# Optimization experiments

Measured on AMD Instinct MI355X. Metric: run time of the kernel, lower is better.

Reference implementation:

```python
import jax, jax.numpy as jnp
import numpy as np

N = 100000      # nodes
D = 128         # embed_dim == hidden_size (code forces them equal)
M = 3           # edge_types / meta-paths
L = 2           # layers
E = 1600000     # edges per meta-path (avg degree 16)
ATT = 128       # semantic attention hidden size


def setup_inputs():
    key = jax.random.key(0)
    ks = jax.random.split(key, 8)
    x = jnp.arange(N)
    edge_index0 = jax.random.randint(ks[0], (2, E), 0, N)
    edge_index1 = jax.random.randint(ks[1], (2, E), 0, N)
    edge_index2 = jax.random.randint(ks[2], (2, E), 0, N)
    embed_table = jax.random.normal(ks[3], (N, D), dtype=jnp.float32) * 0.02
    W = jax.random.normal(ks[4], (L, M, D, D), dtype=jnp.float32) / np.sqrt(D)
    B = jnp.zeros((L, M, D), dtype=jnp.float32)
    att_w1 = jax.random.normal(ks[5], (L, D, ATT), dtype=jnp.float32) / np.sqrt(D)
    att_b1 = jnp.zeros((L, ATT), dtype=jnp.float32)
    att_w2 = jax.random.normal(ks[6], (L, ATT, 1), dtype=jnp.float32) / np.sqrt(ATT)
    return dict(x=x, edge_index0=edge_index0, edge_index1=edge_index1,
                edge_index2=edge_index2, embed_table=embed_table, W=W, B=B,
                att_w1=att_w1, att_b1=att_b1, att_w2=att_w2)


def _gcn_conv(h, W, b, src, dst):
    # GCNConv(normalize=True): self-loops already appended to src/dst.
    deg = jax.ops.segment_sum(jnp.ones_like(dst, dtype=h.dtype), dst, num_segments=N)
    dinv = jnp.where(deg > 0, jax.lax.rsqrt(deg), 0.0)
    norm = dinv[src] * dinv[dst]                       # [E+N]
    hw = h @ W                                         # [N, D]
    msg = hw[src] * norm[:, None]                      # gather + scale
    return jax.ops.segment_sum(msg, dst, num_segments=N) + b


def reference(x, edge_index0, edge_index1, edge_index2,
              embed_table, W, B, att_w1, att_b1, att_w2):
    edges = [edge_index0, edge_index1, edge_index2]
    loops = jnp.arange(N)
    srcs = [jnp.concatenate([e[0], loops]) for e in edges]
    dsts = [jnp.concatenate([e[1], loops]) for e in edges]

    h = embed_table[x]                                 # [N, D]
    for l in range(L):
        sems = [_gcn_conv(h, W[l, m], B[l, m], srcs[m], dsts[m]) for m in range(M)]
        z = jnp.stack(sems, axis=1)                    # [N, M, D]
        # semantic attention: Linear -> tanh -> Linear(no bias), softmax over M
        w = jnp.tanh(z @ att_w1[l] + att_b1[l]) @ att_w2[l]   # [N, M, 1]
        beta = jax.nn.softmax(w, axis=1)
        h = (beta * z).sum(axis=1)                     # [N, D]
    return jax.nn.log_softmax(h, axis=1)
```

## Files before the change

### kernel.cpp

```cpp
#include <hip/hip_runtime.h>
#include <hip/hip_bf16.h>

#define NN 100000
#define DD 128
#define MM 3
#define EE 1600000
#define CH_NODES 512
#define NC ((NN + CH_NODES - 1) / CH_NODES)
#define ECAP 10752
#define ECHTOT ((size_t)NC * ECAP)
#define TILE_E 8192
#define NTILES ((EE + TILE_E - 1) / TILE_E)
#define DTILE 2048
#define NT2 ((NN + DTILE - 1) / DTILE)
#define NT2P 52
#define DBINS 512
#define HSCALE 64.0f
#define HINV (1.0f / 64.0f)
#define PADMARK 0xFFFFFFFFu

typedef unsigned int uint32_hip;
typedef short short8 __attribute__((ext_vector_type(8)));
typedef float floatx4 __attribute__((ext_vector_type(4)));
typedef float floatx2 __attribute__((ext_vector_type(2)));

__device__ __forceinline__ float bf2f(short s) {
  return __uint_as_float(((uint32_hip)(unsigned short)s) << 16);
}
__device__ __forceinline__ unsigned short f2bf(float f) {
  union { __hip_bfloat16 b; unsigned short u; } cv;
  cv.b = __float2bfloat16(f);
  return cv.u;
}
__device__ __forceinline__ uint32_hip packbf2(float x, float y) {
  return (uint32_hip)f2bf(x) | ((uint32_hip)f2bf(y) << 16);
}
__device__ __forceinline__ float tanh_apx(float x) {
  float e = __expf(2.0f * x);
  return 1.0f - 2.0f / (e + 1.0f);
}
__device__ __forceinline__ uint32_hip pack_fp8x4(float a, float b, float c, float d) {
  uint32_hip w = 0;
  w = __builtin_amdgcn_cvt_pk_fp8_f32(a, b, w, false);
  w = __builtin_amdgcn_cvt_pk_fp8_f32(c, d, w, true);
  return w;
}
__device__ __forceinline__ float h2f(uint32_hip u) {
  union { unsigned short us; _Float16 h; } cv;
  cv.us = (unsigned short)u;
  return (float)cv.h;
}
__device__ __forceinline__ unsigned short f2h(float f) {
  union { unsigned short us; _Float16 h; } cv;
  cv.h = (_Float16)f;
  return cv.us;
}
__device__ __forceinline__ void dec16(uint4 hv, floatx2* f) {
  f[0] = __builtin_amdgcn_cvt_pk_f32_fp8((int)hv.x, false);
  f[1] = __builtin_amdgcn_cvt_pk_f32_fp8((int)hv.x, true);
  f[2] = __builtin_amdgcn_cvt_pk_f32_fp8((int)hv.y, false);
  f[3] = __builtin_amdgcn_cvt_pk_f32_fp8((int)hv.y, true);
  f[4] = __builtin_amdgcn_cvt_pk_f32_fp8((int)hv.z, false);
  f[5] = __builtin_amdgcn_cvt_pk_f32_fp8((int)hv.z, true);
  f[6] = __builtin_amdgcn_cvt_pk_f32_fp8((int)hv.w, false);
  f[7] = __builtin_amdgcn_cvt_pk_f32_fp8((int)hv.w, true);
}

__global__ __launch_bounds__(256) void hist1_kernel(const int* __restrict__ e0,
                                                    const int* __restrict__ e1,
                                                    const int* __restrict__ e2,
                                                    int* __restrict__ thist) {
  __shared__ int hist[NC];
  int m = blockIdx.y, tile = blockIdx.x, t = threadIdx.x;
  const int* ei = (m == 0) ? e0 : (m == 1) ? e1 : e2;
  const int* dst = ei + EE;
  int beg = tile * TILE_E, end = min(beg + TILE_E, EE);
  if (t < NC) hist[t] = 0;
  __syncthreads();
  for (int e = beg + t; e < end; e += 256) atomicAdd(&hist[dst[e] >> 9], 1);
  __syncthreads();
  int* th = thist + (size_t)m * NC * NTILES + tile;
  if (t < NC) th[(size_t)t * NTILES] = hist[t];
}

__global__ __launch_bounds__(256) void scan1_kernel(int* __restrict__ thist,
                                                    int* __restrict__ ccount) {
  __shared__ int sw[256];
  int c = blockIdx.x, m = blockIdx.y, t = threadIdx.x;
  int* th = thist + ((size_t)m * NC + c) * NTILES;
  int v = (t < NTILES) ? th[t] : 0;
  sw[t] = v;
  __syncthreads();
  for (int off = 1; off < 256; off <<= 1) {
    int u = (t >= off) ? sw[t - off] : 0;
    __syncthreads();
    sw[t] += u;
    __syncthreads();
  }
  if (t < NTILES) th[t] = c * ECAP + sw[t] - v;
  if (t == NTILES - 1) ccount[m * NC + c] = sw[t];
}

__global__ __launch_bounds__(256) void scatter1_kernel(const int* __restrict__ e0,
                                                       const int* __restrict__ e1,
                                                       const int* __restrict__ e2,
                                                       const int* __restrict__ thist,
                                                       const int* __restrict__ ccount,
                                                       uint32_hip* __restrict__ lvl1) {
  __shared__ int gbase[NC];
  __shared__ int spos[NC];
  __shared__ int cur[NC];
  __shared__ int sw[256];
  __shared__ uint32_hip sval[TILE_E];
  __shared__ unsigned char sbuk[TILE_E];
  int m = blockIdx.y, tile = blockIdx.x, t = threadIdx.x;
  const int* ei = (m == 0) ? e0 : (m == 1) ? e1 : e2;
  const int* dst = ei + EE;
  const int* th = thist + (size_t)m * NC * NTILES + tile;
  int cnt = 0;
  if (t < NC) {
    int gb = th[(size_t)t * NTILES];
    int gn = (tile + 1 < NTILES) ? th[(size_t)t * NTILES + 1] : t * ECAP + ccount[m * NC + t];
    gbase[t] = gb;
    cnt = gn - gb;
  }
  sw[t] = cnt;
  __syncthreads();
  for (int off = 1; off < 256; off <<= 1) {
    int u = (t >= off) ? sw[t - off] : 0;
    __syncthreads();
    sw[t] += u;
    __syncthreads();
  }
  if (t < NC) {
    spos[t] = sw[t] - cnt;
    cur[t] = sw[t] - cnt;
  }
  __syncthreads();
  int beg = tile * TILE_E, end = min(beg + TILE_E, EE);
  int ct = end - beg;
  for (int e = beg + t; e < end; e += 256) {
    int s = ei[e], d = dst[e];
    int b = d >> 9;
    int r = atomicAdd(&cur[b], 1);
    sval[r] = (uint32_hip)s | ((uint32_hip)(d & 511) << 17);
    sbuk[r] = (unsigned char)b;
  }
  __syncthreads();
  uint32_hip* eb = lvl1 + (size_t)m * ECHTOT;
  for (int i = t; i < ct; i += 256) {
    int b = sbuk[i];
    eb[gbase[b] + (i - spos[b])] = sval[i];
  }
}

__global__ __launch_bounds__(256) void sort2_kernel(uint32_hip* __restrict__ lvl1,
                                                    const int* __restrict__ ccount,
                                                    int* __restrict__ astart,
                                                    unsigned short* __restrict__ sdeg,
                                                    int* __restrict__ cpad) {
  __shared__ uint32_hip ebl[ECAP];
  __shared__ int cnt[CH_NODES];
  __shared__ int pos[CH_NODES];
  __shared__ int sw[256];
  int m = blockIdx.y, c = blockIdx.x, t = threadIdx.x;
  int base = c * ECAP;
  int ct = ccount[m * NC + c];
  uint32_hip* eb = lvl1 + (size_t)m * ECHTOT + base;
  for (int e = t; e < ct; e += 256) ebl[e] = eb[e];
  cnt[t] = 0;
  cnt[t + 256] = 0;
  __syncthreads();
  for (int e = t; e < ct; e += 256) atomicAdd(&cnt[ebl[e] >> 17], 1);
  __syncthreads();
  int c0 = cnt[2 * t], c1 = cnt[2 * t + 1];
  int p0 = (c0 + 3) & ~3, p1 = (c1 + 3) & ~3;
  int s = p0 + p1;
  sw[t] = s;
  __syncthreads();
  for (int off = 1; off < 256; off <<= 1) {
    int u = (t >= off) ? sw[t - off] : 0;
    __syncthreads();
    sw[t] += u;
    __syncthreads();
  }
  int excl = sw[t] - s;
  pos[2 * t] = excl;
  pos[2 * t + 1] = excl + p0;
  int node0 = c * CH_NODES;
  {
    int n0 = node0 + 2 * t;
    if (n0 < NN) {
      astart[(size_t)m * NN + n0] = base + excl;
      sdeg[(size_t)m * NN + n0] = (unsigned short)c0;
    }
    int n1 = node0 + 2 * t + 1;
    if (n1 < NN) {
      astart[(size_t)m * NN + n1] = base + excl + p0;
      sdeg[(size_t)m * NN + n1] = (unsigned short)c1;
    }
  }
  if (t == 255) cpad[m * NC + c] = sw[255];
  __syncthreads();
  for (int e = t; e < ct; e += 256) {
    uint32_hip p = ebl[e];
    int q = atomicAdd(&pos[p >> 17], 1);
    eb[q] = p & 0x1FFFFu;
  }
  for (int i = c0; i < p0; ++i) eb[excl + i] = PADMARK;
  for (int i = c1; i < p1; ++i) eb[excl + p0 + i] = PADMARK;
}

__global__ void norm_embed_kernel(uint32_hip* __restrict__ lvl1, const int* __restrict__ cpad,
                                  const unsigned short* __restrict__ sdeg) {
  int m = blockIdx.y, c = blockIdx.x, t = threadIdx.x;
  int base = c * ECAP;
  int ct = cpad[m * NC + c];
  uint32_hip* eb = lvl1 + (size_t)m * ECHTOT + base;
  const unsigned short* sd = sdeg + (size_t)m * NN;
  for (int e = t; e < ct; e += 256) {
    uint32_hip p = eb[e];
    uint32_hip s = p & 0x1FFFFu;
    uint32_hip sc_ = (s < NN) ? s : 0;
    float dv = rsqrtf((float)(sd[sc_] + 1));
    eb[e] = (p == PADMARK) ? 0u : (s | ((uint32_hip)f2h(dv) << 17));
  }
}

__global__ __launch_bounds__(256) void dhist_kernel(const unsigned short* __restrict__ sdeg,
                                                    int* __restrict__ dthist) {
  __shared__ int hist[DBINS];
  int m = blockIdx.y, tile = blockIdx.x, t = threadIdx.x;
  const unsigned short* sd = sdeg + (size_t)m * NN;
  hist[t] = 0;
  hist[t + 256] = 0;
  __syncthreads();
  int beg = tile * DTILE, end = min(beg + DTILE, NN);
  for (int n = beg + t; n < end; n += 256) atomicAdd(&hist[min((int)sd[n], DBINS - 1)], 1);
  __syncthreads();
  int* th = dthist + ((size_t)m * DBINS) * NT2P + tile;
  th[(size_t)t * NT2P] = hist[t];
  th[(size_t)(t + 256) * NT2P] = hist[t + 256];
}

__global__ __launch_bounds__(64) void dscan_kernel(int* __restrict__ dthist,
                                                   int* __restrict__ bintot) {
  __shared__ int sw[64];
  int bin = blockIdx.x, m = blockIdx.y, t = threadIdx.x;
  int* th = dthist + ((size_t)m * DBINS + bin) * NT2P;
  int v = (t < NT2) ? th[t] : 0;
  sw[t] = v;
  __syncthreads();
  for (int off = 1; off < 64; off <<= 1) {
    int u = (t >= off) ? sw[t - off] : 0;
    __syncthreads();
    sw[t] += u;
    __syncthreads();
  }
  if (t < NT2) th[t] = sw[t] - v;
  if (t == 63) bintot[m * DBINS + bin] = sw[63];
}

__global__ __launch_bounds__(512) void dscan2_kernel(const int* __restrict__ bintot,
                                                     int* __restrict__ binbase) {
  __shared__ int sw[DBINS];
  int m = blockIdx.x, t = threadIdx.x;
  int v = bintot[m * DBINS + t];
  sw[t] = v;
  __syncthreads();
  for (int off = 1; off < DBINS; off <<= 1) {
    int u = (t >= off) ? sw[t - off] : 0;
    __syncthreads();
    sw[t] += u;
    __syncthreads();
  }
  binbase[m * DBINS + t] = sw[t] - v;
}

__global__ __launch_bounds__(256) void dscatter_kernel(const unsigned short* __restrict__ sdeg,
                                                       const int* __restrict__ astart,
                                                       const int* __restrict__ dthist,
                                                       const int* __restrict__ binbase,
                                                       uint2* __restrict__ pinfo) {
  __shared__ int cur[DBINS];
  int m = blockIdx.y, tile = blockIdx.x, t = threadIdx.x;
  const unsigned short* sd = sdeg + (size_t)m * NN;
  const int* as_ = astart + (size_t)m * NN;
  for (int b = t; b < DBINS; b += 256)
    cur[b] = binbase[m * DBINS + b] + dthist[((size_t)m * DBINS + b) * NT2P + tile];
  __syncthreads();
  uint2* pi = pinfo + (size_t)m * NN;
  int beg = tile * DTILE, end = min(beg + DTILE, NN);
  for (int n = beg + t; n < end; n += 256) {
    int d = sd[n];
    int r = atomicAdd(&cur[min(d, DBINS - 1)], 1);
    int slot = NN - 1 - r;
    uint2 v;
    v.x = (uint32_hip)as_[n];
    v.y = (uint32_hip)n | ((uint32_hip)d << 17);
    pi[slot] = v;
  }
}

__global__ void embed_kernel(const int* __restrict__ x, const float* __restrict__ tbl,
                             uint32_hip* __restrict__ hq) {
  int i = blockIdx.x * 256 + threadIdx.x;
  if (i < NN * 32) {
    int n = i >> 5;
    int c = i & 31;
    float4 v = ((const float4*)tbl)[(size_t)x[n] * 32 + c];
    hq[(size_t)n * 32 + c] =
        pack_fp8x4(v.x * HSCALE, v.y * HSCALE, v.z * HSCALE, v.w * HSCALE);
  }
}

__global__ __launch_bounds__(256) void agg_kernel(const uint32_hip* __restrict__ hq,
                                                  const uint2* __restrict__ pinfo,
                                                  const uint32_hip* __restrict__ csr,
                                                  uint32_hip* __restrict__ zall) {
  int m = blockIdx.y;
  const uint2* pi_ = pinfo + (size_t)m * NN;
  const uint32_hip* cs = csr + (size_t)m * ECHTOT;
  uint32_hip* zo = zall + (size_t)m * NN * 64;
  int t = threadIdx.x;
  int wave = t >> 6, lane = t & 63;
  int g = lane >> 3, l = lane & 7;
  int slot = blockIdx.x * 32 + wave * 8 + g;
  uint2 pi = pi_[slot];
  int e = (int)pi.x;
  int n = (int)(pi.y & 0x1FFFFu);
  int deg = (int)(pi.y >> 17);
  float di = rsqrtf((float)(deg + 1));
  floatx2 ac[8];
  {
    uint4 hv = *(const uint4*)(hq + (size_t)n * 32 + l * 4);
    floatx2 f[8];
    dec16(hv, f);
    floatx2 di2 = {di, di};
#pragma unroll
    for (int j = 0; j < 8; ++j) ac[j] = di2 * f[j];
  }
  int end = e + ((deg + 3) & ~3);
  uint4 ce = *(const uint4*)(cs + e);
  while (__any(e < end)) {
    int en = e + 4;
    uint4 cn = *(const uint4*)(cs + en);
    uint32_hip msk = (e < end) ? 0xFFFFFFFFu : 0u;
    uint32_hip cearr[4] = {ce.x & msk, ce.y & msk, ce.z & msk, ce.w & msk};
#pragma unroll
    for (int k = 0; k < 4; ++k) {
      uint32_hip ck = cearr[k];
      float nk = h2f(ck >> 17);
      int sk = ck & 0x1FFFF;
      uint4 hk = *(const uint4*)(hq + (size_t)sk * 32 + l * 4);
      floatx2 fk[8];
      dec16(hk, fk);
      floatx2 n2 = {nk, nk};
#pragma unroll
      for (int j = 0; j < 8; ++j) ac[j] = __builtin_elementwise_fma(n2, fk[j], ac[j]);
    }
    ce = cn;
    e = en;
  }
  float scv = di * HINV;
  floatx2 sc2 = {scv, scv};
#pragma unroll
  for (int j = 0; j < 8; ++j) ac[j] = ac[j] * sc2;
  uint4 w0, w1;
  w0.x = packbf2(ac[0].x, ac[0].y);
  w0.y = packbf2(ac[1].x, ac[1].y);
  w0.z = packbf2(ac[2].x, ac[2].y);
  w0.w = packbf2(ac[3].x, ac[3].y);
  w1.x = packbf2(ac[4].x, ac[4].y);
  w1.y = packbf2(ac[5].x, ac[5].y);
  w1.z = packbf2(ac[6].x, ac[6].y);
  w1.w = packbf2(ac[7].x, ac[7].y);
  uint32_hip* zr = zo + (size_t)n * 64 + l * 8;
  *(uint4*)zr = w0;
  *(uint4*)(zr + 4) = w1;
}

__global__ __launch_bounds__(256) void mfma_gemm_kernel(unsigned short* __restrict__ zall,
                                                        const float* __restrict__ Wall,
                                                        const float* __restrict__ Ball) {
  __shared__ unsigned short Wt[128 * 136];
  int m = blockIdx.y;
  const float* Wmat = Wall + (size_t)m * DD * DD;
  const float* bias = Ball + (size_t)m * DD;
  unsigned short* Z = zall + (size_t)m * NN * DD;
  int t = threadIdx.x;
  {
    uint32_hip* Wt_u = (uint32_hip*)Wt;
#pragma unroll
    for (int i = 0; i < 32; ++i) {
      int idx = i * 256 + t;
      int k2 = idx >> 7;
      int nn = idx & 127;
      float w0 = Wmat[(2 * k2) * 128 + nn];
      float w1 = Wmat[(2 * k2 + 1) * 128 + nn];
      Wt_u[nn * 68 + k2] = packbf2(w0, w1);
    }
  }
  __syncthreads();
  int wave = t >> 6, lane = t & 63;
  int quad = lane >> 4, ln = lane & 15;
  int rowbase = blockIdx.x * 64 + wave * 16;
  int arow = rowbase + ln;
  int arowc = (arow < NN) ? arow : (NN - 1);
  const short8* zrow = (const short8*)(Z + (size_t)arowc * 128);
  floatx4 acc[8];
#pragma unroll
  for (int c = 0; c < 8; ++c) acc[c] = (floatx4){0.f, 0.f, 0.f, 0.f};
#pragma unroll
  for (int kt = 0; kt < 4; ++kt) {
    short8 a = zrow[kt * 4 + quad];
#pragma unroll
    for (int c = 0; c < 8; ++c) {
      const short8* bp = (const short8*)(Wt + (c * 16 + ln) * 136 + kt * 32 + quad * 8);
      acc[c] = __builtin_amdgcn_mfma_f32_16x16x32_bf16(a, *bp, acc[c], 0, 0, 0);
    }
  }
#pragma unroll
  for (int c = 0; c < 8; ++c) {
    int col = c * 16 + ln;
    float bs = bias[col];
#pragma unroll
    for (int r = 0; r < 4; ++r) {
      int grow = rowbase + quad * 4 + r;
      if (grow < NN) Z[(size_t)grow * 128 + col] = f2bf(acc[c][r] + bs);
    }
  }
}

__global__ __launch_bounds__(256) void att_combine_kernel(
    const unsigned short* __restrict__ Z, const float* __restrict__ W1,
    const float* __restrict__ b1, const float* __restrict__ w2,
    uint32_hip* __restrict__ hq, float* __restrict__ fout, int last) {
  __shared__ unsigned short Wt[128 * 136];
  __shared__ float sc[4][3][16];
  int t = threadIdx.x;
  {
    uint32_hip* Wt_u = (uint32_hip*)Wt;
#pragma unroll
    for (int i = 0; i < 32; ++i) {
      int idx = i * 256 + t;
      int k2 = idx >> 7;
      int nn = idx & 127;
      float w0 = W1[(2 * k2) * 128 + nn];
      float w1 = W1[(2 * k2 + 1) * 128 + nn];
      Wt_u[nn * 68 + k2] = packbf2(w0, w1);
    }
  }
  __syncthreads();
  int wave = t >> 6, lane = t & 63;
  int quad = lane >> 4, ln = lane & 15;
  int nodebase = blockIdx.x * 64 + wave * 16;
  int frow = nodebase + ln;
  int frowc = (frow < NN) ? frow : (NN - 1);
  short8 af[3][4];
#pragma unroll
  for (int m = 0; m < 3; ++m) {
    const short8* zr = (const short8*)(Z + ((size_t)m * NN + frowc) * 128);
#pragma unroll
    for (int kt = 0; kt < 4; ++kt) af[m][kt] = zr[kt * 4 + quad];
  }
#pragma unroll
  for (int m = 0; m < 3; ++m) {
    floatx4 acc[8];
#pragma unroll
    for (int c = 0; c < 8; ++c) acc[c] = (floatx4){0.f, 0.f, 0.f, 0.f};
#pragma unroll
    for (int kt = 0; kt < 4; ++kt) {
#pragma unroll
      for (int c = 0; c < 8; ++c) {
        const short8* bp = (const short8*)(Wt + (c * 16 + ln) * 136 + kt * 32 + quad * 8);
        acc[c] = __builtin_amdgcn_mfma_f32_16x16x32_bf16(af[m][kt], *bp, acc[c], 0, 0, 0);
      }
    }
    float rows[4] = {0.f, 0.f, 0.f, 0.f};
#pragma unroll
    for (int c = 0; c < 8; ++c) {
      int col = c * 16 + ln;
      float bb = b1[col];
      float ww = w2[col];
#pragma unroll
      for (int r = 0; r < 4; ++r) rows[r] += tanh_apx(acc[c][r] + bb) * ww;
    }
#pragma unroll
    for (int off = 8; off > 0; off >>= 1) {
#pragma unroll
      for (int r = 0; r < 4; ++r) rows[r] += __shfl_down(rows[r], off);
    }
    if (ln == 0) {
#pragma unroll
      for (int r = 0; r < 4; ++r) sc[wave][m][quad * 4 + r] = rows[r];
    }
  }
  __syncthreads();
  float s0 = sc[wave][0][ln], s1 = sc[wave][1][ln], s2 = sc[wave][2][ln];
  float mx = fmaxf(s0, fmaxf(s1, s2));
  float e0 = __expf(s0 - mx), e1 = __expf(s1 - mx), e2 = __expf(s2 - mx);
  float inv = 1.0f / (e0 + e1 + e2);
  float bb0 = e0 * inv, bb1 = e1 * inv, bb2 = e2 * inv;
  float o[4][8];
#pragma unroll
  for (int kt = 0; kt < 4; ++kt) {
#pragma unroll
    for (int j = 0; j < 8; ++j) {
      o[kt][j] = bb0 * bf2f(af[0][kt][j]) + bb1 * bf2f(af[1][kt][j]) + bb2 * bf2f(af[2][kt][j]);
    }
  }
  if (!last) {
    if (frow < NN) {
#pragma unroll
      for (int kt = 0; kt < 4; ++kt) {
        uint2 v;
        v.x = pack_fp8x4(o[kt][0] * HSCALE, o[kt][1] * HSCALE, o[kt][2] * HSCALE,
                         o[kt][3] * HSCALE);
        v.y = pack_fp8x4(o[kt][4] * HSCALE, o[kt][5] * HSCALE, o[kt][6] * HSCALE,
                         o[kt][7] * HSCALE);
        *(uint2*)&hq[(size_t)frow * 32 + kt * 8 + quad * 2] = v;
      }
    }
  } else {
    float vmx = o[0][0];
#pragma unroll
    for (int kt = 0; kt < 4; ++kt)
#pragma unroll
      for (int j = 0; j < 8; ++j) vmx = fmaxf(vmx, o[kt][j]);
    vmx = fmaxf(vmx, __shfl_xor(vmx, 16));
    vmx = fmaxf(vmx, __shfl_xor(vmx, 32));
    float ss = 0.f;
#pragma unroll
    for (int kt = 0; kt < 4; ++kt)
#pragma unroll
      for (int j = 0; j < 8; ++j) ss += __expf(o[kt][j] - vmx);
    ss += __shfl_xor(ss, 16);
    ss += __shfl_xor(ss, 32);
    float lse = vmx + logf(ss);
    if (frow < NN) {
#pragma unroll
      for (int kt = 0; kt < 4; ++kt) {
        float4 a, b;
        a.x = o[kt][0] - lse; a.y = o[kt][1] - lse; a.z = o[kt][2] - lse; a.w = o[kt][3] - lse;
        b.x = o[kt][4] - lse; b.y = o[kt][5] - lse; b.z = o[kt][6] - lse; b.w = o[kt][7] - lse;
        float* dst = fout + (size_t)frow * 128 + kt * 32 + quad * 8;
        *(float4*)dst = a;
        *(float4*)(dst + 4) = b;
      }
    }
  }
}

extern "C" void kernel_launch(void* const* d_in, const int* in_sizes, int n_in,
                              void* d_out, int out_size, void* d_ws, size_t ws_size,
                              hipStream_t stream) {
  const int* x = (const int*)d_in[0];
  const int* e0 = (const int*)d_in[1];
  const int* e1 = (const int*)d_in[2];
  const int* e2 = (const int*)d_in[3];
  const float* embed = (const float*)d_in[4];
  const float* W = (const float*)d_in[5];
  const float* B = (const float*)d_in[6];
  const float* aw1 = (const float*)d_in[7];
  const float* ab1 = (const float*)d_in[8];
  const float* aw2 = (const float*)d_in[9];
  float* out = (float*)d_out;
  uint32_hip* hq = (uint32_hip*)d_out;

  char* ws = (char*)d_ws;
  size_t off = 0;
  auto alloc = [&](size_t bytes) {
    void* p = ws + off;
    off += (bytes + 255) & ~(size_t)255;
    return p;
  };
  unsigned short* z = (unsigned short*)alloc((size_t)MM * NN * DD * 2);
  uint32_hip* lvl1 = (uint32_hip*)alloc((size_t)MM * ECHTOT * 4 + 4096);
  int* astart = (int*)alloc((size_t)MM * NN * 4);
  unsigned short* sdeg = (unsigned short*)alloc((size_t)MM * NN * 2);
  int* ccount = (int*)alloc((size_t)MM * NC * 4);
  int* cpad = (int*)alloc((size_t)MM * NC * 4);
  uint2* pinfo = (uint2*)alloc((size_t)MM * NN * 8);
  int* thist = (int*)alloc((size_t)MM * NC * NTILES * 4);
  int* dthist = (int*)alloc((size_t)MM * DBINS * NT2P * 4);
  int* bintot = (int*)alloc((size_t)MM * DBINS * 4);
  int* binbase = (int*)alloc((size_t)MM * DBINS * 4);

  dim3 bs(256);
  hist1_kernel<<<dim3(NTILES, 3), bs, 0, stream>>>(e0, e1, e2, thist);
  scan1_kernel<<<dim3(NC, 3), bs, 0, stream>>>(thist, ccount);
  scatter1_kernel<<<dim3(NTILES, 3), bs, 0, stream>>>(e0, e1, e2, thist, ccount, lvl1);
  sort2_kernel<<<dim3(NC, 3), bs, 0, stream>>>(lvl1, ccount, astart, sdeg, cpad);
  norm_embed_kernel<<<dim3(NC, 3), bs, 0, stream>>>(lvl1, cpad, sdeg);
  dhist_kernel<<<dim3(NT2, 3), bs, 0, stream>>>(sdeg, dthist);
  dscan_kernel<<<dim3(DBINS, 3), dim3(64), 0, stream>>>(dthist, bintot);
  dscan2_kernel<<<dim3(3), dim3(DBINS), 0, stream>>>(bintot, binbase);
  dscatter_kernel<<<dim3(NT2, 3), bs, 0, stream>>>(sdeg, astart, dthist, binbase, pinfo);
  embed_kernel<<<dim3((NN * 32 + 255) / 256), bs, 0, stream>>>(x, embed, hq);

  for (int l = 0; l < 2; ++l) {
    agg_kernel<<<dim3(NN / 32, 3), bs, 0, stream>>>(
        (const uint32_hip*)hq, pinfo, lvl1, (uint32_hip*)z);
    mfma_gemm_kernel<<<dim3((NN + 63) / 64, 3), bs, 0, stream>>>(
        z, W + (size_t)l * 3 * DD * DD, B + (size_t)l * 3 * DD);
    att_combine_kernel<<<dim3((NN + 63) / 64), bs, 0, stream>>>(
        z, aw1 + (size_t)l * DD * DD, ab1 + (size_t)l * DD, aw2 + (size_t)l * DD, hq, out, l == 1);
  }
}
```

Baseline: 654.9 us.

## Fuse GCN aggregation with weight GEMM and pre-convert weights to bf16 once

The separate aggregation and MFMA GEMM kernels are merged. Each block now aggregates 32 nodes into a shared-memory bf16 tile and multiplies it by W directly, which removes a full write and re-read of the intermediate z buffer for all three meta-paths. A new prep kernel transposes and converts all W and attention W1 matrices to bf16 once, so the GEMM and attention kernels read B fragments from global/L2 instead of rebuilding an LDS copy in every block. The costs are one extra barrier in the aggregation kernel, scattered row writes indexed by the degree-sorted node ids, and B operands loaded from global memory rather than LDS.

```diff
diff --git a/kernel.cpp b/kernel.cpp
--- a/kernel.cpp
+++ b/kernel.cpp
@@ -64,6 +64,18 @@
   f[5] = __builtin_amdgcn_cvt_pk_f32_fp8((int)hv.z, true);
   f[6] = __builtin_amdgcn_cvt_pk_f32_fp8((int)hv.w, false);
   f[7] = __builtin_amdgcn_cvt_pk_f32_fp8((int)hv.w, true);
+}
+
+__global__ __launch_bounds__(256) void wprep_kernel(const float* __restrict__ W,
+                                                    const float* __restrict__ aw1,
+                                                    unsigned short* __restrict__ wbf) {
+  int tot = blockIdx.x * 256 + threadIdx.x;
+  int mat = tot >> 14;
+  int i = tot & 16383;
+  int n = i >> 7, k = i & 127;
+  float v = (mat < 6) ? W[(size_t)mat * 16384 + k * 128 + n]
+                      : aw1[(size_t)(mat - 6) * 16384 + k * 128 + n];
+  wbf[tot] = f2bf(v);
 }
 
 __global__ __launch_bounds__(256) void hist1_kernel(const int* __restrict__ e0,
@@ -314,14 +326,15 @@
   }
 }
 
-__global__ __launch_bounds__(256) void agg_kernel(const uint32_hip* __restrict__ hq,
-                                                  const uint2* __restrict__ pinfo,
-                                                  const uint32_hip* __restrict__ csr,
-                                                  uint32_hip* __restrict__ zall) {
+__global__ __launch_bounds__(256) void agg_gemm_kernel(
+    const uint32_hip* __restrict__ hq, const uint2* __restrict__ pinfo,
+    const uint32_hip* __restrict__ csr, const unsigned short* __restrict__ wbf,
+    const float* __restrict__ Ball, unsigned short* __restrict__ zall) {
+  __shared__ unsigned short ztile[32][136];
+  __shared__ int nid[32];
   int m = blockIdx.y;
   const uint2* pi_ = pinfo + (size_t)m * NN;
   const uint32_hip* cs = csr + (size_t)m * ECHTOT;
-  uint32_hip* zo = zall + (size_t)m * NN * 64;
   int t = threadIdx.x;
   int wave = t >> 6, lane = t & 63;
   int g = lane >> 3, l = lane & 7;
@@ -330,6 +343,8 @@
   int e = (int)pi.x;
   int n = (int)(pi.y & 0x1FFFFu);
   int deg = (int)(pi.y >> 17);
+  int row = wave * 8 + g;
+  if (l == 0) nid[row] = n;
   float di = rsqrtf((float)(deg + 1));
   floatx2 ac[8];
   {
@@ -375,83 +390,44 @@
   w1.y = packbf2(ac[5].x, ac[5].y);
   w1.z = packbf2(ac[6].x, ac[6].y);
   w1.w = packbf2(ac[7].x, ac[7].y);
-  uint32_hip* zr = zo + (size_t)n * 64 + l * 8;
-  *(uint4*)zr = w0;
-  *(uint4*)(zr + 4) = w1;
-}
-
-__global__ __launch_bounds__(256) void mfma_gemm_kernel(unsigned short* __restrict__ zall,
-                                                        const float* __restrict__ Wall,
-                                                        const float* __restrict__ Ball) {
-  __shared__ unsigned short Wt[128 * 136];
-  int m = blockIdx.y;
-  const float* Wmat = Wall + (size_t)m * DD * DD;
+  *(uint4*)&ztile[row][l * 16] = w0;
+  *(uint4*)&ztile[row][l * 16 + 8] = w1;
+  __syncthreads();
+  int rt = wave & 1, ch = wave >> 1;
+  int quad = lane >> 4, ln = lane & 15;
+  const unsigned short* wb = wbf + (size_t)m * (DD * DD);
   const float* bias = Ball + (size_t)m * DD;
+  floatx4 acc[4];
+#pragma unroll
+  for (int c = 0; c < 4; ++c) acc[c] = (floatx4){0.f, 0.f, 0.f, 0.f};
+#pragma unroll
+  for (int kt = 0; kt < 4; ++kt) {
+    short8 a = *(const short8*)&ztile[rt * 16 + ln][kt * 32 + quad * 8];
+#pragma unroll
+    for (int c = 0; c < 4; ++c) {
+      short8 b = *(const short8*)(wb + (size_t)(ch * 64 + c * 16 + ln) * DD + kt * 32 + quad * 8);
+      acc[c] = __builtin_amdgcn_mfma_f32_16x16x32_bf16(a, b, acc[c], 0, 0, 0);
+    }
+  }
   unsigned short* Z = zall + (size_t)m * NN * DD;
-  int t = threadIdx.x;
-  {
-    uint32_hip* Wt_u = (uint32_hip*)Wt;
-#pragma unroll
-    for (int i = 0; i < 32; ++i) {
-      int idx = i * 256 + t;
-      int k2 = idx >> 7;
-      int nn = idx & 127;
-      float w0 = Wmat[(2 * k2) * 128 + nn];
-      float w1 = Wmat[(2 * k2 + 1) * 128 + nn];
-      Wt_u[nn * 68 + k2] = packbf2(w0, w1);
-    }
-  }
-  __syncthreads();
-  int wave = t >> 6, lane = t & 63;
-  int quad = lane >> 4, ln = lane & 15;
-  int rowbase = blockIdx.x * 64 + wave * 16;
-  int arow = rowbase + ln;
-  int arowc = (arow < NN) ? arow : (NN - 1);
-  const short8* zrow = (const short8*)(Z + (size_t)arowc * 128);
-  floatx4 acc[8];
-#pragma unroll
-  for (int c = 0; c < 8; ++c) acc[c] = (floatx4){0.f, 0.f, 0.f, 0.f};
-#pragma unroll
-  for (int kt = 0; kt < 4; ++kt) {
-    short8 a = zrow[kt * 4 + quad];
-#pragma unroll
-    for (int c = 0; c < 8; ++c) {
-      const short8* bp = (const short8*)(Wt + (c * 16 + ln) * 136 + kt * 32 + quad * 8);
-      acc[c] = __builtin_amdgcn_mfma_f32_16x16x32_bf16(a, *bp, acc[c], 0, 0, 0);
-    }
-  }
-#pragma unroll
-  for (int c = 0; c < 8; ++c) {
-    int col = c * 16 + ln;
+#pragma unroll
+  for (int c = 0; c < 4; ++c) {
+    int col = ch * 64 + c * 16 + ln;
     float bs = bias[col];
 #pragma unroll
     for (int r = 0; r < 4; ++r) {
-      int grow = rowbase + quad * 4 + r;
-      if (grow < NN) Z[(size_t)grow * 128 + col] = f2bf(acc[c][r] + bs);
+      int node = nid[rt * 16 + quad * 4 + r];
+      Z[(size_t)node * DD + col] = f2bf(acc[c][r] + bs);
     }
   }
 }
 
 __global__ __launch_bounds__(256) void att_combine_kernel(
-    const unsigned short* __restrict__ Z, const float* __restrict__ W1,
+    const unsigned short* __restrict__ Z, const unsigned short* __restrict__ wb1,
     const float* __restrict__ b1, const float* __restrict__ w2,
     uint32_hip* __restrict__ hq, float* __restrict__ fout, int last) {
-  __shared__ unsigned short Wt[128 * 136];
   __shared__ float sc[4][3][16];
   int t = threadIdx.x;
-  {
-    uint32_hip* Wt_u = (uint32_hip*)Wt;
-#pragma unroll
-    for (int i = 0; i < 32; ++i) {
-      int idx = i * 256 + t;
-      int k2 = idx >> 7;
-      int nn = idx & 127;
-      float w0 = W1[(2 * k2) * 128 + nn];
-      float w1 = W1[(2 * k2 + 1) * 128 + nn];
-      Wt_u[nn * 68 + k2] = packbf2(w0, w1);
-    }
-  }
-  __syncthreads();
   int wave = t >> 6, lane = t & 63;
   int quad = lane >> 4, ln = lane & 15;
   int nodebase = blockIdx.x * 64 + wave * 16;
@@ -473,8 +449,9 @@
     for (int kt = 0; kt < 4; ++kt) {
 #pragma unroll
       for (int c = 0; c < 8; ++c) {
-        const short8* bp = (const short8*)(Wt + (c * 16 + ln) * 136 + kt * 32 + quad * 8);
-        acc[c] = __builtin_amdgcn_mfma_f32_16x16x32_bf16(af[m][kt], *bp, acc[c], 0, 0, 0);
+        short8 b =
+            *(const short8*)(wb1 + (size_t)(c * 16 + ln) * DD + kt * 32 + quad * 8);
+        acc[c] = __builtin_amdgcn_mfma_f32_16x16x32_bf16(af[m][kt], b, acc[c], 0, 0, 0);
       }
     }
     float rows[4] = {0.f, 0.f, 0.f, 0.f};
@@ -586,8 +563,10 @@
   int* dthist = (int*)alloc((size_t)MM * DBINS * NT2P * 4);
   int* bintot = (int*)alloc((size_t)MM * DBINS * 4);
   int* binbase = (int*)alloc((size_t)MM * DBINS * 4);
+  unsigned short* wbf = (unsigned short*)alloc((size_t)8 * DD * DD * 2);
 
   dim3 bs(256);
+  wprep_kernel<<<dim3(512), bs, 0, stream>>>(W, aw1, wbf);
   hist1_kernel<<<dim3(NTILES, 3), bs, 0, stream>>>(e0, e1, e2, thist);
   scan1_kernel<<<dim3(NC, 3), bs, 0, stream>>>(thist, ccount);
   scatter1_kernel<<<dim3(NTILES, 3), bs, 0, stream>>>(e0, e1, e2, thist, ccount, lvl1);
@@ -600,11 +579,11 @@
   embed_kernel<<<dim3((NN * 32 + 255) / 256), bs, 0, stream>>>(x, embed, hq);
 
   for (int l = 0; l < 2; ++l) {
-    agg_kernel<<<dim3(NN / 32, 3), bs, 0, stream>>>(
-        (const uint32_hip*)hq, pinfo, lvl1, (uint32_hip*)z);
-    mfma_gemm_kernel<<<dim3((NN + 63) / 64, 3), bs, 0, stream>>>(
-        z, W + (size_t)l * 3 * DD * DD, B + (size_t)l * 3 * DD);
+    agg_gemm_kernel<<<dim3(NN / 32, 3), bs, 0, stream>>>(
+        (const uint32_hip*)hq, pinfo, lvl1, wbf + (size_t)l * 3 * DD * DD,
+        B + (size_t)l * 3 * DD, (unsigned short*)z);
     att_combine_kernel<<<dim3((NN + 63) / 64), bs, 0, stream>>>(
-        z, aw1 + (size_t)l * DD * DD, ab1 + (size_t)l * DD, aw2 + (size_t)l * DD, hq, out, l == 1);
-  }
-}
+        z, wbf + (size_t)(6 + l) * DD * DD, ab1 + (size_t)l * DD, aw2 + (size_t)l * DD,
+        hq, out, l == 1);
+  }
+}
```

Result: slower. 743.4 us (+13.5%).
